# Optimization experiments

Hardware: AMD Instinct MI355X
Metric: run time of the kernel (lower is better)

The kernel has to match this reference:

```python
import jax, jax.numpy as jnp
import numpy as np

N, E, R = 50000, 1600000, 8
IN_F, HID_F, OUT_F = 128, 64, 64


def setup_inputs() -> dict:
    key = jax.random.key(0)
    ks = jax.random.split(key, 9)
    x = jax.random.normal(ks[0], (N, IN_F), dtype=jnp.float32)
    edge_index = jax.random.randint(ks[1], (2, E), 0, N, dtype=jnp.int64)
    edge_type = jax.random.randint(ks[2], (E,), 0, R, dtype=jnp.int64)
    # layer 1 params (scaled like glorot)
    s1 = 1.0 / np.sqrt(IN_F)
    W1_rel = jax.random.normal(ks[3], (R, IN_F, HID_F), dtype=jnp.float32) * s1
    W1_root = jax.random.normal(ks[4], (IN_F, HID_F), dtype=jnp.float32) * s1
    b1 = jnp.zeros((HID_F,), dtype=jnp.float32)
    # layer 2 params
    s2 = 1.0 / np.sqrt(HID_F)
    W2_rel = jax.random.normal(ks[5], (R, HID_F, OUT_F), dtype=jnp.float32) * s2
    W2_root = jax.random.normal(ks[6], (HID_F, OUT_F), dtype=jnp.float32) * s2
    b2 = jnp.zeros((OUT_F,), dtype=jnp.float32)
    return {"x": x, "edge_index": edge_index, "edge_type": edge_type,
            "W1_rel": W1_rel, "W1_root": W1_root, "b1": b1,
            "W2_rel": W2_rel, "W2_root": W2_root, "b2": b2}


def _rgcn_conv(x, src, dst, etype, W_rel, W_root, b):
    """PyG RGCNConv: root transform + per-relation mean-aggregated messages."""
    n = x.shape[0]
    r = W_rel.shape[0]
    # per-relation transform of all node features: [R, N, H]
    xw = jnp.einsum('nd,rdh->rnh', x, W_rel)
    # per-edge message: transformed source feature under the edge's relation
    msg = xw[etype, src]  # [E, H]
    # mean normalization per (dst, relation) pair
    key = dst * r + etype  # [E]
    cnt = jax.ops.segment_sum(jnp.ones(etype.shape, dtype=x.dtype), key,
                              num_segments=n * r)
    inv = 1.0 / jnp.maximum(cnt, 1.0)
    msg = msg * inv[key][:, None]
    # scatter-add into target nodes
    agg = jax.ops.segment_sum(msg, dst, num_segments=n)  # [N, H]
    return agg + x @ W_root + b


def reference(x, edge_index, edge_type, W1_rel, W1_root, b1, W2_rel, W2_root, b2):
    src, dst = edge_index[0], edge_index[1]
    h = _rgcn_conv(x, src, dst, edge_type, W1_rel, W1_root, b1)
    h = jax.nn.relu(h)
    out = _rgcn_conv(h, src, dst, edge_type, W2_rel, W2_root, b2)
    return out
```

## Files before the change

### kernel.cpp

```cpp
#include <hip/hip_runtime.h>


constexpr int NN  = 50000;
constexpr int NE  = 1600000;
constexpr int NR  = 8;
constexpr int FIN = 128;
constexpr int FH  = 64;

constexpr int BSH = 7;
constexpr int BN  = 1 << BSH;
constexpr int NB  = (NN + BN - 1) >> BSH;
constexpr int CAP = 6144;
constexpr int CH  = 4096;
constexpr int NAPP = (NE + CH - 1) / CH;
constexpr unsigned XWMAX = (unsigned)(NN - 1) * (NR * 64) + (NR - 1) * 64;

typedef __attribute__((ext_vector_type(8))) short bf16x8;
typedef __attribute__((ext_vector_type(4))) float f32x4;

__device__ __forceinline__ unsigned short f2bf(float f) {
  unsigned u = __float_as_uint(f);
  u = (u + 0x7fff + ((u >> 16) & 1)) >> 16;
  return (unsigned short)u;
}
__device__ __forceinline__ float bf2f(unsigned short b) {
  return __uint_as_float(((unsigned)b) << 16);
}
__device__ __forceinline__ bool edge_ok(unsigned s, unsigned d, unsigned r) {
  return s < NN && d < NN && r < NR;
}

__device__ void append_body(char* smem, int bx,
                            const int* __restrict__ src,
                            const int* __restrict__ dst,
                            const int* __restrict__ et,
                            int* __restrict__ bcur,
                            unsigned* __restrict__ brecs) {
  uint2* stage = (uint2*)smem;
  int* h     = (int*)(smem + (size_t)CH * 8);
  int* gbase = h + NB;
  int* sbase = gbase + NB;
  int* scur  = sbase + NB;
  int* wtot  = scur + NB;

  const int t  = threadIdx.x;
  const int c0 = bx * CH;
  const int m  = min(CH, NE - c0);

  for (int i = t; i < NB; i += 256) h[i] = 0;
  __syncthreads();

  for (int i = t; i < m; i += 256) {
    const unsigned s = (unsigned)src[c0 + i];
    const unsigned d = (unsigned)dst[c0 + i];
    const unsigned r = (unsigned)et[c0 + i];
    if (edge_ok(s, d, r)) atomicAdd(&h[d >> BSH], 1);
  }
  __syncthreads();

  const int v0 = (2 * t < NB) ? h[2 * t] : 0;
  const int v1 = (2 * t + 1 < NB) ? h[2 * t + 1] : 0;
  if (2 * t < NB     && v0) gbase[2 * t]     = atomicAdd(&bcur[2 * t], v0);
  if (2 * t + 1 < NB && v1) gbase[2 * t + 1] = atomicAdd(&bcur[2 * t + 1], v1);
  const int s = v0 + v1;
  int incl = s;
#pragma unroll
  for (int o = 1; o < 64; o <<= 1) {
    int u = __shfl_up(incl, o, 64);
    if ((t & 63) >= o) incl += u;
  }
  if ((t & 63) == 63) wtot[t >> 6] = incl;
  __syncthreads();
  int wo = 0;
  for (int w = 0; w < (t >> 6); ++w) wo += wtot[w];
  const int e = wo + incl - s;
  if (2 * t < NB)     { sbase[2 * t] = e;          scur[2 * t] = e; }
  if (2 * t + 1 < NB) { sbase[2 * t + 1] = e + v0; scur[2 * t + 1] = e + v0; }
  __syncthreads();

  for (int i = t; i < m; i += 256) {
    const unsigned sv = (unsigned)src[c0 + i];
    const unsigned d  = (unsigned)dst[c0 + i];
    const unsigned r  = (unsigned)et[c0 + i];
    if (edge_ok(sv, d, r)) {
      const int p = atomicAdd(&scur[d >> BSH], 1);
      if (p < CH) stage[p] = make_uint2((sv << 10) | (((unsigned)d & (BN - 1)) << 3) | r, d);
    }
  }
  __syncthreads();

  const int M = min(sbase[NB - 1] + h[NB - 1], CH);
  for (int j = t; j < M; j += 256) {
    const uint2 rec = stage[j];
    const int b = (int)(rec.y >> BSH);
    const int idx = min(gbase[b] + (j - sbase[b]), NB * CAP - 1);
    brecs[idx] = rec.x;
  }
}

__global__ void __launch_bounds__(256) bucket_finalize(
    const int* __restrict__ bcur, const unsigned* __restrict__ brecs,
    int* __restrict__ row_start, int* __restrict__ deg,
    unsigned* __restrict__ recs) {
  const int b    = blockIdx.x;
  const int base = b * CAP;
  const int m    = min(bcur[b] - base, CAP);
  const int d0   = b << BSH;
  __shared__ int cnt[BN * NR];
  __shared__ int curs[BN * NR];
  __shared__ int wtot[4];
  const int t = threadIdx.x;

  for (int i = t; i < BN * NR; i += 256) cnt[i] = 0;
  __syncthreads();
  for (int i = t; i < m; i += 256) {
    const unsigned rec = brecs[base + i];
    const int dl = (int)((rec >> 3) & (BN - 1));
    const int r  = (int)(rec & 7);
    atomicAdd(&cnt[dl * NR + r], 1);
  }
  __syncthreads();

  const int c0 = cnt[t * 4], c1 = cnt[t * 4 + 1], c2 = cnt[t * 4 + 2], c3 = cnt[t * 4 + 3];
  const int s = c0 + c1 + c2 + c3;
  int incl = s;
#pragma unroll
  for (int o = 1; o < 64; o <<= 1) {
    int u = __shfl_up(incl, o, 64);
    if ((t & 63) >= o) incl += u;
  }
  if ((t & 63) == 63) wtot[t >> 6] = incl;
  __syncthreads();
  int wo = 0;
  for (int w = 0; w < (t >> 6); ++w) wo += wtot[w];
  const int e = wo + incl - s;
  curs[t * 4]     = e;
  curs[t * 4 + 1] = e + c0;
  curs[t * 4 + 2] = e + c0 + c1;
  curs[t * 4 + 3] = e + c0 + c1 + c2;
  __syncthreads();

  if (t < BN) {
    const int d = d0 + t;
    if (d < NN) {
      const int start = curs[t * NR];
      const int end   = (t == BN - 1) ? m : curs[(t + 1) * NR];
      row_start[d] = base + start;
      deg[d]       = end - start;
    }
  }
  __syncthreads();

  for (int i = t; i < m; i += 256) {
    const unsigned rec = brecs[base + i];
    const int dl = (int)((rec >> 3) & (BN - 1));
    const int r  = (int)(rec & 7);
    const unsigned sv = rec >> 10;
    const int p  = atomicAdd(&curs[dl * NR + r], 1);
    const unsigned cn = (unsigned)min(cnt[dl * NR + r], 127);
    recs[base + min(p, CAP - 1)] = (cn << 25) | (sv << 9) | ((unsigned)r << 6);
  }
}

__global__ void prep(const float* __restrict__ W1r, const float* __restrict__ W1o,
                     const float* __restrict__ W2r, const float* __restrict__ W2o,
                     unsigned short* __restrict__ Wt1,
                     unsigned short* __restrict__ Wt2,
                     int* __restrict__ bcur) {
  const int i  = blockIdx.x * blockDim.x + threadIdx.x;
  if (i < NB) bcur[i] = i * CAP;
  const int n1 = (NR + 1) * 64 * FIN;
  const int n2 = (NR + 1) * 64 * FH;
  if (i < n1) {
    const int g = i / (64 * FIN), rem = i % (64 * FIN);
    const int n = rem / FIN, k = rem % FIN;
    const float* W = (g < NR) ? (W1r + (size_t)g * FIN * 64) : W1o;
    Wt1[i] = f2bf(W[k * 64 + n]);
  } else if (i < n1 + n2) {
    const int j = i - n1;
    const int g = j / (64 * FH), rem = j % (64 * FH);
    const int n = rem / FH, k = rem % FH;
    const float* W = (g < NR) ? (W2r + (size_t)g * FH * 64) : W2o;
    Wt2[j] = f2bf(W[k * 64 + n]);
  }
}

template <int K, bool A_FP32>
__device__ void gemm_body(char* smem, int bx,
                          const void* __restrict__ Av,
                          const unsigned short* __restrict__ Wt,
                          const float* __restrict__ bias,
                          unsigned short* __restrict__ xw,
                          float* __restrict__ root_out) {
  constexpr int KP  = K + 8;
  constexpr int NCH = 64 * (K / 8) / 256;
  unsigned short* As  = (unsigned short*)smem;
  unsigned short* Bs0 = As + 64 * KP;
  const int n0  = bx * 64;
  const int tid = threadIdx.x;

  if constexpr (A_FP32) {
    const float* A = (const float*)Av;
    for (int c = tid; c < 64 * (K / 8); c += 256) {
      const int row = c / (K / 8), kp = (c % (K / 8)) * 8;
      bf16x8 v = {};
      if (n0 + row < NN) {
        const float* p = A + (size_t)(n0 + row) * K + kp;
        const float4 f0 = *(const float4*)p;
        const float4 f1 = *(const float4*)(p + 4);
        v[0] = f2bf(f0.x); v[1] = f2bf(f0.y); v[2] = f2bf(f0.z); v[3] = f2bf(f0.w);
        v[4] = f2bf(f1.x); v[5] = f2bf(f1.y); v[6] = f2bf(f1.z); v[7] = f2bf(f1.w);
      }
      *(bf16x8*)(As + row * KP + kp) = v;
    }
  } else {
    const unsigned short* A = (const unsigned short*)Av;
    for (int c = tid; c < 64 * (K / 8); c += 256) {
      const int row = c / (K / 8), kp = (c % (K / 8)) * 8;
      bf16x8 v = {};
      if (n0 + row < NN) v = *(const bf16x8*)(A + (size_t)(n0 + row) * K + kp);
      *(bf16x8*)(As + row * KP + kp) = v;
    }
  }

  for (int c = 0; c < NCH; ++c) {
    const int idx = tid + c * 256;
    const int row = idx / (K / 8), kp = (idx % (K / 8)) * 8;
    *(bf16x8*)(Bs0 + row * KP + kp) = *(const bf16x8*)(Wt + idx * 8);
  }
  __syncthreads();

  const int wave = tid >> 6, lane = tid & 63;
  const int i16 = lane & 15, quad = lane >> 4;
  const int r0 = wave * 16 + i16;

  for (int g = 0; g <= NR; ++g) {
    const int buf = g & 1;
    unsigned short* Bc = Bs0 + buf * 64 * KP;
    unsigned short* Bn = Bs0 + (buf ^ 1) * 64 * KP;
    bf16x8 breg[NCH];
    if (g < NR) {
      const unsigned short* Wn = Wt + (size_t)(g + 1) * 64 * K;
#pragma unroll
      for (int c = 0; c < NCH; ++c) breg[c] = *(const bf16x8*)(Wn + (tid + c * 256) * 8);
    }

    f32x4 acc[4] = {};
#pragma unroll
    for (int kc = 0; kc < K / 32; ++kc) {
      const int k0 = kc * 32 + quad * 8;
      const bf16x8 a0 = *(const bf16x8*)(As + r0 * KP + k0);
      const bf16x8 b0 = *(const bf16x8*)(Bc + (i16)      * KP + k0);
      const bf16x8 b1 = *(const bf16x8*)(Bc + (i16 + 16) * KP + k0);
      const bf16x8 b2 = *(const bf16x8*)(Bc + (i16 + 32) * KP + k0);
      const bf16x8 b3 = *(const bf16x8*)(Bc + (i16 + 48) * KP + k0);
      acc[0] = __builtin_amdgcn_mfma_f32_16x16x32_bf16(a0, b0, acc[0], 0, 0, 0);
      acc[1] = __builtin_amdgcn_mfma_f32_16x16x32_bf16(a0, b1, acc[1], 0, 0, 0);
      acc[2] = __builtin_amdgcn_mfma_f32_16x16x32_bf16(a0, b2, acc[2], 0, 0, 0);
      acc[3] = __builtin_amdgcn_mfma_f32_16x16x32_bf16(a0, b3, acc[3], 0, 0, 0);
    }

    if (g < NR) {
#pragma unroll
      for (int c = 0; c < NCH; ++c) {
        const int idx = tid + c * 256;
        const int row = idx / (K / 8), kp = (idx % (K / 8)) * 8;
        *(bf16x8*)(Bn + row * KP + kp) = breg[c];
      }
    }

    if (g < NR) {
#pragma unroll
      for (int reg = 0; reg < 4; ++reg) {
        const int n = n0 + wave * 16 + quad * 4 + reg;
        if (n >= NN) continue;
        unsigned short* p = xw + (size_t)n * (NR * 64) + g * 64 + i16;
#pragma unroll
        for (int ct = 0; ct < 4; ++ct) p[ct * 16] = f2bf(acc[ct][reg]);
      }
    } else {
      float bv[4];
#pragma unroll
      for (int ct = 0; ct < 4; ++ct) bv[ct] = bias[ct * 16 + i16];
#pragma unroll
      for (int reg = 0; reg < 4; ++reg) {
        const int n = n0 + wave * 16 + quad * 4 + reg;
        if (n >= NN) continue;
        float* p = root_out + (size_t)n * 64 + i16;
#pragma unroll
        for (int ct = 0; ct < 4; ++ct) p[ct * 16] = acc[ct][reg] + bv[ct];
      }
    }
    __syncthreads();
  }
}

__global__ void __launch_bounds__(256) fused_append_gemm1(
    const int* __restrict__ src, const int* __restrict__ dst,
    const int* __restrict__ et, int* __restrict__ bcur,
    unsigned* __restrict__ brecs,
    const float* __restrict__ A, const unsigned short* __restrict__ Wt,
    const float* __restrict__ bias, unsigned short* __restrict__ xw,
    float* __restrict__ root_out) {
  extern __shared__ char smem[];
  if ((int)blockIdx.x < NAPP)
    append_body(smem, (int)blockIdx.x, src, dst, et, bcur, brecs);
  else
    gemm_body<FIN, true>(smem, (int)blockIdx.x - NAPP, A, Wt, bias, xw, root_out);
}

__global__ void __launch_bounds__(256) gemm_l2(
    const unsigned short* __restrict__ A, const unsigned short* __restrict__ Wt,
    const float* __restrict__ bias, unsigned short* __restrict__ xw,
    float* __restrict__ out) {
  extern __shared__ char smem[];
  gemm_body<FH, false>(smem, (int)blockIdx.x, A, Wt, bias, xw, out);
}

template <bool RELU_BF16>
__global__ void __launch_bounds__(256) agg_csr(
    const int* __restrict__ row_start, const int* __restrict__ deg,
    const unsigned* __restrict__ recs, const unsigned short* __restrict__ xw,
    const float* __restrict__ root,
    float* __restrict__ out_f32, unsigned short* __restrict__ out_b16) {
  const int gid  = blockIdx.x * blockDim.x + threadIdx.x;
  const int lane = gid & 63;
  const int d    = gid >> 6;
  if (d >= NN) return;
  const int e  = lane >> 3;
  const int l8 = lane & 7;
  const int base = row_start[d];
  const int n    = deg[d];
  const unsigned* po = recs + base;
  const unsigned short* xp = xw + l8 * 8;
  float a[8] = {};

  for (int i0 = 0; i0 < n; i0 += 32) {
    const int i = i0 + e;
    const unsigned r0 = (i      < n) ? po[i]      : 0u;
    const unsigned r1 = (i + 8  < n) ? po[i + 8]  : 0u;
    const unsigned r2 = (i + 16 < n) ? po[i + 16] : 0u;
    const unsigned r3 = (i + 24 < n) ? po[i + 24] : 0u;
    const unsigned u0 = min(r0 & 0x01FFFFFFu, XWMAX);
    const unsigned u1 = min(r1 & 0x01FFFFFFu, XWMAX);
    const unsigned u2 = min(r2 & 0x01FFFFFFu, XWMAX);
    const unsigned u3 = min(r3 & 0x01FFFFFFu, XWMAX);
    const bf16x8 v0 = *(const bf16x8*)(xp + u0);
    const bf16x8 v1 = *(const bf16x8*)(xp + u1);
    const bf16x8 v2 = *(const bf16x8*)(xp + u2);
    const bf16x8 v3 = *(const bf16x8*)(xp + u3);
    float w0 = __builtin_amdgcn_rcpf((float)(r0 >> 25));
    float w1 = __builtin_amdgcn_rcpf((float)(r1 >> 25));
    float w2 = __builtin_amdgcn_rcpf((float)(r2 >> 25));
    float w3 = __builtin_amdgcn_rcpf((float)(r3 >> 25));
    if (i      >= n) w0 = 0.f;
    if (i + 8  >= n) w1 = 0.f;
    if (i + 16 >= n) w2 = 0.f;
    if (i + 24 >= n) w3 = 0.f;
#pragma unroll
    for (int q = 0; q < 8; ++q) a[q] += bf2f((unsigned short)v0[q]) * w0;
#pragma unroll
    for (int q = 0; q < 8; ++q) a[q] += bf2f((unsigned short)v1[q]) * w1;
#pragma unroll
    for (int q = 0; q < 8; ++q) a[q] += bf2f((unsigned short)v2[q]) * w2;
#pragma unroll
    for (int q = 0; q < 8; ++q) a[q] += bf2f((unsigned short)v3[q]) * w3;
  }

#pragma unroll
  for (int q = 0; q < 8; ++q) {
    a[q] += __shfl_xor(a[q], 8, 64);
    a[q] += __shfl_xor(a[q], 16, 64);
    a[q] += __shfl_xor(a[q], 32, 64);
  }

  if (e == 0) {
    const float4 r0 = *(const float4*)(root + (size_t)d * 64 + l8 * 8);
    const float4 r1 = *(const float4*)(root + (size_t)d * 64 + l8 * 8 + 4);
    const float o[8] = {r0.x + a[0], r0.y + a[1], r0.z + a[2], r0.w + a[3],
                        r1.x + a[4], r1.y + a[5], r1.z + a[6], r1.w + a[7]};
    if (RELU_BF16) {
      bf16x8 ov;
#pragma unroll
      for (int q = 0; q < 8; ++q) ov[q] = (short)f2bf(fmaxf(o[q], 0.f));
      *(bf16x8*)(out_b16 + (size_t)d * 64 + l8 * 8) = ov;
    } else {
      *(float4*)(out_f32 + (size_t)d * 64 + l8 * 8)     = make_float4(o[0], o[1], o[2], o[3]);
      *(float4*)(out_f32 + (size_t)d * 64 + l8 * 8 + 4) = make_float4(o[4], o[5], o[6], o[7]);
    }
  }
}

extern "C" void kernel_launch(void* const* d_in, const int* in_sizes, int n_in,
                              void* d_out, int out_size, void* d_ws, size_t ws_size,
                              hipStream_t stream) {
  const float* x   = (const float*)d_in[0];
  const int*   ei  = (const int*)d_in[1];
  const int*   et  = (const int*)d_in[2];
  const float* W1r = (const float*)d_in[3];
  const float* W1o = (const float*)d_in[4];
  const float* b1  = (const float*)d_in[5];
  const float* W2r = (const float*)d_in[6];
  const float* W2o = (const float*)d_in[7];
  const float* b2  = (const float*)d_in[8];
  float* out = (float*)d_out;

  const int* src = ei;
  const int* dst = ei + NE;

  char* ws = (char*)d_ws;
  size_t off = 0;
  auto alloc = [&](size_t bytes) {
    void* p = ws + off; off += (bytes + 255) & ~(size_t)255; return p;
  };
  int*   bcur      = (int*)alloc((size_t)NB * 4);
  int*   row_start = (int*)alloc((size_t)NN * 4);
  int*   deg       = (int*)alloc((size_t)NN * 4);
  unsigned* brecs  = (unsigned*)alloc((size_t)NB * CAP * 4);
  unsigned* offs   = (unsigned*)alloc((size_t)NB * CAP * 4);
  unsigned short* xw    = (unsigned short*)alloc((size_t)NN * NR * 64 * 2);
  unsigned short* hb    = (unsigned short*)alloc((size_t)NN * FH * 2);
  float*          hroot = (float*)alloc((size_t)NN * 64 * 4);
  unsigned short* Wt1   = (unsigned short*)alloc((size_t)(NR + 1) * 64 * FIN * 2);
  unsigned short* Wt2   = (unsigned short*)alloc((size_t)(NR + 1) * 64 * FH * 2);

  const int nprep = (NR + 1) * 64 * (FIN + FH);
  prep<<<(nprep + 255) / 256, 256, 0, stream>>>(W1r, W1o, W2r, W2o, Wt1, Wt2, bcur);

  const int gemm_blocks = (NN + 63) / 64;
  const int agg_blocks  = (NN * 64 + 255) / 256;
  constexpr int SM1 = 3 * 64 * (FIN + 8) * 2;
  constexpr int SM2 = 3 * 64 * (FH + 8) * 2;

  fused_append_gemm1<<<NAPP + gemm_blocks, 256, SM1, stream>>>(
      src, dst, et, bcur, brecs, x, Wt1, b1, xw, hroot);
  bucket_finalize<<<NB, 256, 0, stream>>>(bcur, brecs, row_start, deg, offs);

  agg_csr<true><<<agg_blocks, 256, 0, stream>>>(row_start, deg, offs, xw, hroot, nullptr, hb);
  gemm_l2<<<gemm_blocks, 256, SM2, stream>>>(hb, Wt2, b2, xw, out);
  agg_csr<false><<<agg_blocks, 256, 0, stream>>>(row_start, deg, offs, xw, out, out, nullptr);
}
```

Before: 243.3 us.

## Keep GEMM A fragments in registers, interleave append/GEMM blocks, deepen aggregation loads

The GEMM body now loads each wave's A-row fragments straight from global memory into registers instead of staging them in LDS. This cuts LDS usage to the double-buffered B tiles, so the layer-2 GEMM and the fused kernel request less shared memory. The fused append+GEMM1 kernel interleaves append blocks with GEMM blocks (one in three) so both kinds of work run at the same time across the GPU. The aggregation loop processes 64 edges per iteration with 8 outstanding gathers, exposing more memory-level parallelism at the cost of extra registers.

```diff
diff --git a/kernel.cpp b/kernel.cpp
--- a/kernel.cpp
+++ b/kernel.cpp
@@ -194,32 +194,37 @@
                           float* __restrict__ root_out) {
   constexpr int KP  = K + 8;
   constexpr int NCH = 64 * (K / 8) / 256;
-  unsigned short* As  = (unsigned short*)smem;
-  unsigned short* Bs0 = As + 64 * KP;
+  constexpr int NKC = K / 32;
+  unsigned short* Bs0 = (unsigned short*)smem;
   const int n0  = bx * 64;
   const int tid = threadIdx.x;
-
+  const int wave = tid >> 6, lane = tid & 63;
+  const int i16 = lane & 15, quad = lane >> 4;
+  const int r0 = wave * 16 + i16;
+  const int arow = n0 + r0;
+
+  bf16x8 afrag[NKC];
   if constexpr (A_FP32) {
     const float* A = (const float*)Av;
-    for (int c = tid; c < 64 * (K / 8); c += 256) {
-      const int row = c / (K / 8), kp = (c % (K / 8)) * 8;
+#pragma unroll
+    for (int kc = 0; kc < NKC; ++kc) {
       bf16x8 v = {};
-      if (n0 + row < NN) {
-        const float* p = A + (size_t)(n0 + row) * K + kp;
+      if (arow < NN) {
+        const float* p = A + (size_t)arow * K + kc * 32 + quad * 8;
         const float4 f0 = *(const float4*)p;
         const float4 f1 = *(const float4*)(p + 4);
         v[0] = f2bf(f0.x); v[1] = f2bf(f0.y); v[2] = f2bf(f0.z); v[3] = f2bf(f0.w);
         v[4] = f2bf(f1.x); v[5] = f2bf(f1.y); v[6] = f2bf(f1.z); v[7] = f2bf(f1.w);
       }
-      *(bf16x8*)(As + row * KP + kp) = v;
+      afrag[kc] = v;
     }
   } else {
     const unsigned short* A = (const unsigned short*)Av;
-    for (int c = tid; c < 64 * (K / 8); c += 256) {
-      const int row = c / (K / 8), kp = (c % (K / 8)) * 8;
+#pragma unroll
+    for (int kc = 0; kc < NKC; ++kc) {
       bf16x8 v = {};
-      if (n0 + row < NN) v = *(const bf16x8*)(A + (size_t)(n0 + row) * K + kp);
-      *(bf16x8*)(As + row * KP + kp) = v;
+      if (arow < NN) v = *(const bf16x8*)(A + (size_t)arow * K + kc * 32 + quad * 8);
+      afrag[kc] = v;
     }
   }
 
@@ -229,10 +234,6 @@
     *(bf16x8*)(Bs0 + row * KP + kp) = *(const bf16x8*)(Wt + idx * 8);
   }
   __syncthreads();
-
-  const int wave = tid >> 6, lane = tid & 63;
-  const int i16 = lane & 15, quad = lane >> 4;
-  const int r0 = wave * 16 + i16;
 
   for (int g = 0; g <= NR; ++g) {
     const int buf = g & 1;
@@ -247,9 +248,9 @@
 
     f32x4 acc[4] = {};
 #pragma unroll
-    for (int kc = 0; kc < K / 32; ++kc) {
+    for (int kc = 0; kc < NKC; ++kc) {
       const int k0 = kc * 32 + quad * 8;
-      const bf16x8 a0 = *(const bf16x8*)(As + r0 * KP + k0);
+      const bf16x8 a0 = afrag[kc];
       const bf16x8 b0 = *(const bf16x8*)(Bc + (i16)      * KP + k0);
       const bf16x8 b1 = *(const bf16x8*)(Bc + (i16 + 16) * KP + k0);
       const bf16x8 b2 = *(const bf16x8*)(Bc + (i16 + 32) * KP + k0);
@@ -267,9 +268,6 @@
         const int row = idx / (K / 8), kp = (idx % (K / 8)) * 8;
         *(bf16x8*)(Bn + row * KP + kp) = breg[c];
       }
-    }
-
-    if (g < NR) {
 #pragma unroll
       for (int reg = 0; reg < 4; ++reg) {
         const int n = n0 + wave * 16 + quad * 4 + reg;
@@ -303,10 +301,11 @@
     const float* __restrict__ bias, unsigned short* __restrict__ xw,
     float* __restrict__ root_out) {
   extern __shared__ char smem[];
-  if ((int)blockIdx.x < NAPP)
-    append_body(smem, (int)blockIdx.x, src, dst, et, bcur, brecs);
+  const int bx = (int)blockIdx.x;
+  if (bx % 3 == 2 && bx / 3 < NAPP)
+    append_body(smem, bx / 3, src, dst, et, bcur, brecs);
   else
-    gemm_body<FIN, true>(smem, (int)blockIdx.x - NAPP, A, Wt, bias, xw, root_out);
+    gemm_body<FIN, true>(smem, bx - (bx + 1) / 3, A, Wt, bias, xw, root_out);
 }
 
 __global__ void __launch_bounds__(256) gemm_l2(
@@ -335,7 +334,29 @@
   const unsigned short* xp = xw + l8 * 8;
   float a[8] = {};
 
-  for (int i0 = 0; i0 < n; i0 += 32) {
+  int i0 = 0;
+  for (; i0 + 32 < n; i0 += 64) {
+    unsigned rr[8];
+#pragma unroll
+    for (int sl = 0; sl < 8; ++sl) {
+      const int i = i0 + e + 8 * sl;
+      rr[sl] = (i < n) ? po[i] : 0u;
+    }
+    bf16x8 vv[8];
+#pragma unroll
+    for (int sl = 0; sl < 8; ++sl) {
+      const unsigned u = min(rr[sl] & 0x01FFFFFFu, XWMAX);
+      vv[sl] = *(const bf16x8*)(xp + u);
+    }
+#pragma unroll
+    for (int sl = 0; sl < 8; ++sl) {
+      float w = __builtin_amdgcn_rcpf((float)(rr[sl] >> 25));
+      if (i0 + e + 8 * sl >= n) w = 0.f;
+#pragma unroll
+      for (int q = 0; q < 8; ++q) a[q] += bf2f((unsigned short)vv[sl][q]) * w;
+    }
+  }
+  if (i0 < n) {
     const int i = i0 + e;
     const unsigned r0 = (i      < n) ? po[i]      : 0u;
     const unsigned r1 = (i + 8  < n) ? po[i + 8]  : 0u;
@@ -429,8 +450,8 @@
 
   const int gemm_blocks = (NN + 63) / 64;
   const int agg_blocks  = (NN * 64 + 255) / 256;
-  constexpr int SM1 = 3 * 64 * (FIN + 8) * 2;
-  constexpr int SM2 = 3 * 64 * (FH + 8) * 2;
+  constexpr int SM1 = CH * 8 + 4 * NB * 4 + 16;
+  constexpr int SM2 = 2 * 64 * (FH + 8) * 2;
 
   fused_append_gemm1<<<NAPP + gemm_blocks, 256, SM1, stream>>>(
       src, dst, et, bcur, brecs, x, Wt1, b1, xw, hroot);
```

New measurement: 239.4 us. About the same (-1.6%).
